# Kernel optimization log

Hardware: AMD Instinct MI355X
Metric: run time of the kernel (lower is better)

## Reference

```python
import jax, jax.numpy as jnp
import numpy as np

NEG_SLOPE = 0.2
EPS = 1e-16


def gat_layer(x, src, dst, W, att_src, att_dst, bias, heads, concat):
    N = x.shape[0]
    C = W.shape[1] // heads
    h = (x @ W).reshape(N, heads, C)                      # [N,H,C]
    a_src = (h * att_src).sum(-1)                         # [N,H]
    a_dst = (h * att_dst).sum(-1)                         # [N,H]
    e = jax.nn.leaky_relu(a_src[src] + a_dst[dst], NEG_SLOPE)  # [E,H]
    # numerically-stable softmax over incoming edges of each dst node
    e_max = jax.ops.segment_max(e, dst, num_segments=N)   # [N,H]
    e_max = jnp.where(jnp.isfinite(e_max), e_max, 0.0)
    ex = jnp.exp(e - e_max[dst])                          # [E,H]
    denom = jax.ops.segment_sum(ex, dst, num_segments=N) + EPS
    alpha = ex / denom[dst]                               # [E,H]
    msg = alpha[:, :, None] * h[src]                      # [E,H,C]
    out = jax.ops.segment_sum(msg, dst, num_segments=N)   # [N,H,C]
    if concat:
        return out.reshape(N, heads * C) + bias
    return out.mean(axis=1) + bias


def setup_inputs() -> dict:
    key = jax.random.key(0)
    ks = jax.random.split(key, 12)
    N, E = 50000, 800000
    IN, HID, OUT, H = 128, 8, 40, 8
    x = jax.random.normal(ks[0], (N, IN), dtype=jnp.float32)
    edge_index = jax.random.randint(ks[1], (2, E), 0, N, dtype=jnp.int64)
    s1 = 1.0 / np.sqrt(IN)
    s2 = 1.0 / np.sqrt(HID * H)
    W1 = jax.random.normal(ks[2], (IN, H * HID), dtype=jnp.float32) * s1
    att_src1 = jax.random.normal(ks[3], (H, HID), dtype=jnp.float32) * 0.1
    att_dst1 = jax.random.normal(ks[4], (H, HID), dtype=jnp.float32) * 0.1
    bias1 = jnp.zeros((H * HID,), dtype=jnp.float32)
    W2 = jax.random.normal(ks[5], (H * HID, OUT), dtype=jnp.float32) * s2
    att_src2 = jax.random.normal(ks[6], (1, OUT), dtype=jnp.float32) * 0.1
    att_dst2 = jax.random.normal(ks[7], (1, OUT), dtype=jnp.float32) * 0.1
    bias2 = jnp.zeros((OUT,), dtype=jnp.float32)
    return {"x": x, "edge_index": edge_index,
            "W1": W1, "att_src1": att_src1, "att_dst1": att_dst1, "bias1": bias1,
            "W2": W2, "att_src2": att_src2, "att_dst2": att_dst2, "bias2": bias2}


def reference(x, edge_index, W1, att_src1, att_dst1, bias1, W2, att_src2, att_dst2, bias2):
    src, dst = edge_index[0], edge_index[1]
    # eval mode: dropout is identity
    h = gat_layer(x, src, dst, W1, att_src1, att_dst1, bias1, heads=8, concat=True)
    h = jax.nn.elu(h)
    out = gat_layer(h, src, dst, W2, att_src2, att_dst2, bias2, heads=1, concat=False)
    return out
```

## Files before the change

### kernel.cpp

```cpp
#include <hip/hip_runtime.h>
#include <math.h>

#define EPS 1e-16f
#define SLOT 64
__device__ __forceinline__ float lrelu(float v) { return v > 0.0f ? v : 0.2f * v; }

__device__ __forceinline__ unsigned short f2bf(float f) {
    unsigned u = __float_as_uint(f);
    u += 0x7FFF + ((u >> 16) & 1);
    return (unsigned short)(u >> 16);
}
__device__ __forceinline__ float bf2f(unsigned short s) {
    return __uint_as_float(((unsigned)s) << 16);
}

__global__ void k_zero(int* __restrict__ deg, int N) {
    int i = blockIdx.x * 256 + threadIdx.x;
    if (i < N) deg[i] = 0;
}

#define LDK1 129
#define LDN1 65
__global__ __launch_bounds__(256, 2) void k_gemm1_scat(
    const float* __restrict__ x, const float* __restrict__ W1,
    const float* __restrict__ att_src1, const float* __restrict__ att_dst1,
    unsigned short* __restrict__ h1b, float* __restrict__ a_src1, float* __restrict__ a_dst1,
    int N, int D, const int* __restrict__ src, const int* __restrict__ dst,
    int* __restrict__ deg, int* __restrict__ ssrc, int E) {
    __shared__ float sX[64 * LDK1];
    __shared__ float sW[128 * LDN1];
    int t = threadIdx.x;
    if (blockIdx.x < D) {
        int e0 = (blockIdx.x * 256 + t) * 4;
        if (e0 < E) {
            int4 s4 = *((const int4*)(src + e0));
            int4 d4 = *((const int4*)(dst + e0));
            int p0 = atomicAdd(&deg[d4.x], 1);
            int p1 = atomicAdd(&deg[d4.y], 1);
            int p2 = atomicAdd(&deg[d4.z], 1);
            int p3 = atomicAdd(&deg[d4.w], 1);
            if (p0 < SLOT) ssrc[(d4.x << 6) + p0] = s4.x;
            if (p1 < SLOT) ssrc[(d4.y << 6) + p1] = s4.y;
            if (p2 < SLOT) ssrc[(d4.z << 6) + p2] = s4.z;
            if (p3 < SLOT) ssrc[(d4.w << 6) + p3] = s4.w;
        }
        return;
    }
    int r0 = (blockIdx.x - D) * 64;
    for (int i = t; i < 2048; i += 256) {
        int k = i >> 4, n4 = i & 15;
        float4 v = ((const float4*)W1)[i];
        float* p = sW + k * LDN1 + 4 * n4;
        p[0] = v.x; p[1] = v.y; p[2] = v.z; p[3] = v.w;
    }
    for (int i = t; i < 2048; i += 256) {
        int m = i >> 5, k4 = i & 31;
        int r = r0 + m;
        float4 v = make_float4(0.f, 0.f, 0.f, 0.f);
        if (r < N) v = ((const float4*)(x + (size_t)r * 128))[k4];
        float* p = sX + m * LDK1 + 4 * k4;
        p[0] = v.x; p[1] = v.y; p[2] = v.z; p[3] = v.w;
    }
    __syncthreads();
    int tx = t & 15, ty = t >> 4;
    const float* pA = sX + 4 * tx * LDK1;
    const float* pB = sW + 4 * ty;
    float c[4][4] = {{0.f}};
#pragma unroll 8
    for (int k = 0; k < 128; k++) {
        float a0 = pA[k], a1 = pA[LDK1 + k], a2 = pA[2 * LDK1 + k], a3 = pA[3 * LDK1 + k];
        const float* pb = pB + k * LDN1;
        float b0 = pb[0], b1 = pb[1], b2 = pb[2], b3 = pb[3];
        c[0][0] = fmaf(a0, b0, c[0][0]); c[0][1] = fmaf(a0, b1, c[0][1]);
        c[0][2] = fmaf(a0, b2, c[0][2]); c[0][3] = fmaf(a0, b3, c[0][3]);
        c[1][0] = fmaf(a1, b0, c[1][0]); c[1][1] = fmaf(a1, b1, c[1][1]);
        c[1][2] = fmaf(a1, b2, c[1][2]); c[1][3] = fmaf(a1, b3, c[1][3]);
        c[2][0] = fmaf(a2, b0, c[2][0]); c[2][1] = fmaf(a2, b1, c[2][1]);
        c[2][2] = fmaf(a2, b2, c[2][2]); c[2][3] = fmaf(a2, b3, c[2][3]);
        c[3][0] = fmaf(a3, b0, c[3][0]); c[3][1] = fmaf(a3, b1, c[3][1]);
        c[3][2] = fmaf(a3, b2, c[3][2]); c[3][3] = fmaf(a3, b3, c[3][3]);
    }
    float as0 = att_src1[4 * ty + 0], as1 = att_src1[4 * ty + 1],
          as2 = att_src1[4 * ty + 2], as3 = att_src1[4 * ty + 3];
    float ad0 = att_dst1[4 * ty + 0], ad1 = att_dst1[4 * ty + 1],
          ad2 = att_dst1[4 * ty + 2], ad3 = att_dst1[4 * ty + 3];
    __syncthreads();
    float* sPs = sX;
    float* sPd = sX + 64 * 17;
#pragma unroll
    for (int i = 0; i < 4; i++) {
        int row = 4 * tx + i;
        int r = r0 + row;
        if (r < N) {
            ushort4 hv;
            hv.x = f2bf(c[i][0]); hv.y = f2bf(c[i][1]);
            hv.z = f2bf(c[i][2]); hv.w = f2bf(c[i][3]);
            *((ushort4*)(h1b + (size_t)r * 64 + 4 * ty)) = hv;
        }
        sPs[row * 17 + ty] = fmaf(c[i][0], as0, fmaf(c[i][1], as1, fmaf(c[i][2], as2, c[i][3] * as3)));
        sPd[row * 17 + ty] = fmaf(c[i][0], ad0, fmaf(c[i][1], ad1, fmaf(c[i][2], ad2, c[i][3] * ad3)));
    }
    __syncthreads();
    for (int i = t; i < 512; i += 256) {
        int row = i >> 3, h = i & 7;
        int r = r0 + row;
        if (r < N) {
            a_src1[r * 8 + h] = sPs[row * 17 + 2 * h] + sPs[row * 17 + 2 * h + 1];
            a_dst1[r * 8 + h] = sPd[row * 17 + 2 * h] + sPd[row * 17 + 2 * h + 1];
        }
    }
}

__global__ __launch_bounds__(256) void k_node_agg1(
    const int* __restrict__ deg, const int* __restrict__ ssrc,
    const float* __restrict__ a_src1, const float* __restrict__ a_dst1,
    const unsigned short* __restrict__ h1b, const float* __restrict__ bias1,
    float* __restrict__ xx, int N) {
    int d = (blockIdx.x * 256 + threadIdx.x) >> 6;
    int lane = threadIdx.x & 63;
    if (d >= N) return;
    int start = d << 6;
    int end = start + min(deg[d], SLOT);
    int hcol = lane >> 3;
    int h8 = lane & 7;
    int eoff = lane >> 3;
    float adst8 = a_dst1[d * 8 + h8];
    float acc0 = 0.0f, acc1 = 0.0f, lsumA = 0.0f;
    int base = start;
    for (; base + 8 <= end; base += 8) {
        int s_l = ssrc[base + eoff];
        float ex_l = __expf(lrelu(a_src1[(size_t)s_l * 8 + h8] + adst8));
        lsumA += ex_l;
        int s0 = __shfl(s_l, 0),  s1 = __shfl(s_l, 8),  s2 = __shfl(s_l, 16), s3 = __shfl(s_l, 24);
        int s4 = __shfl(s_l, 32), s5 = __shfl(s_l, 40), s6 = __shfl(s_l, 48), s7 = __shfl(s_l, 56);
        float f0 = __shfl(ex_l, hcol),      f1 = __shfl(ex_l, 8 + hcol);
        float f2 = __shfl(ex_l, 16 + hcol), f3 = __shfl(ex_l, 24 + hcol);
        float f4 = __shfl(ex_l, 32 + hcol), f5 = __shfl(ex_l, 40 + hcol);
        float f6 = __shfl(ex_l, 48 + hcol), f7 = __shfl(ex_l, 56 + hcol);
        float g0 = bf2f(h1b[(size_t)s0 * 64 + lane]), g1 = bf2f(h1b[(size_t)s1 * 64 + lane]);
        float g2 = bf2f(h1b[(size_t)s2 * 64 + lane]), g3 = bf2f(h1b[(size_t)s3 * 64 + lane]);
        float g4 = bf2f(h1b[(size_t)s4 * 64 + lane]), g5 = bf2f(h1b[(size_t)s5 * 64 + lane]);
        float g6 = bf2f(h1b[(size_t)s6 * 64 + lane]), g7 = bf2f(h1b[(size_t)s7 * 64 + lane]);
        acc0 = fmaf(f0, g0, acc0); acc1 = fmaf(f1, g1, acc1);
        acc0 = fmaf(f2, g2, acc0); acc1 = fmaf(f3, g3, acc1);
        acc0 = fmaf(f4, g4, acc0); acc1 = fmaf(f5, g5, acc1);
        acc0 = fmaf(f6, g6, acc0); acc1 = fmaf(f7, g7, acc1);
    }
    int ecnt = end - base;
    if (ecnt > 0) {
        int s_l = 0; float ex_l = 0.0f;
        if (eoff < ecnt) {
            s_l = ssrc[base + eoff];
            ex_l = __expf(lrelu(a_src1[(size_t)s_l * 8 + h8] + adst8));
        }
        lsumA += ex_l;
        for (int j = 0; j < ecnt; j++) {
            int sj = __shfl(s_l, j * 8);
            float fj = __shfl(ex_l, j * 8 + hcol);
            acc0 = fmaf(fj, bf2f(h1b[(size_t)sj * 64 + lane]), acc0);
        }
    }
    float t = lsumA;
    t += __shfl_xor(t, 8); t += __shfl_xor(t, 16); t += __shfl_xor(t, 32);
    float lsum = __shfl(t, hcol);
    float o = (acc0 + acc1) / (lsum + EPS) + bias1[lane];
    xx[(size_t)d * 64 + lane] = o > 0.0f ? o : expm1f(o);
}

#define LDK2 65
#define LDN2 41
__global__ __launch_bounds__(256, 2) void k_gemm2(
    const float* __restrict__ xx, const float* __restrict__ W2,
    const float* __restrict__ att_src2, const float* __restrict__ att_dst2,
    float* __restrict__ h2, float* __restrict__ a_src2, float* __restrict__ a_dst2, int N) {
    __shared__ float sX[64 * LDK2];
    __shared__ float sW[64 * LDN2];
    int t = threadIdx.x;
    int r0 = blockIdx.x * 64;
    for (int i = t; i < 640; i += 256) {
        int k = i / 10, n4 = i - k * 10;
        float4 v = ((const float4*)W2)[i];
        float* p = sW + k * LDN2 + 4 * n4;
        p[0] = v.x; p[1] = v.y; p[2] = v.z; p[3] = v.w;
    }
    for (int i = t; i < 1024; i += 256) {
        int m = i >> 4, k4 = i & 15;
        int r = r0 + m;
        float4 v = make_float4(0.f, 0.f, 0.f, 0.f);
        if (r < N) v = ((const float4*)(xx + (size_t)r * 64))[k4];
        float* p = sX + m * LDK2 + 4 * k4;
        p[0] = v.x; p[1] = v.y; p[2] = v.z; p[3] = v.w;
    }
    __syncthreads();
    int tx = t & 15, ty = t >> 4;
    bool act = ty < 10;
    float c[4][4] = {{0.f}};
    if (act) {
        const float* pA = sX + 4 * tx * LDK2;
        const float* pB = sW + 4 * ty;
#pragma unroll 8
        for (int k = 0; k < 64; k++) {
            float a0 = pA[k], a1 = pA[LDK2 + k], a2 = pA[2 * LDK2 + k], a3 = pA[3 * LDK2 + k];
            const float* pb = pB + k * LDN2;
            float b0 = pb[0], b1 = pb[1], b2 = pb[2], b3 = pb[3];
            c[0][0] = fmaf(a0, b0, c[0][0]); c[0][1] = fmaf(a0, b1, c[0][1]);
            c[0][2] = fmaf(a0, b2, c[0][2]); c[0][3] = fmaf(a0, b3, c[0][3]);
            c[1][0] = fmaf(a1, b0, c[1][0]); c[1][1] = fmaf(a1, b1, c[1][1]);
            c[1][2] = fmaf(a1, b2, c[1][2]); c[1][3] = fmaf(a1, b3, c[1][3]);
            c[2][0] = fmaf(a2, b0, c[2][0]); c[2][1] = fmaf(a2, b1, c[2][1]);
            c[2][2] = fmaf(a2, b2, c[2][2]); c[2][3] = fmaf(a2, b3, c[2][3]);
            c[3][0] = fmaf(a3, b0, c[3][0]); c[3][1] = fmaf(a3, b1, c[3][1]);
            c[3][2] = fmaf(a3, b2, c[3][2]); c[3][3] = fmaf(a3, b3, c[3][3]);
        }
    }
    float as0 = 0.f, as1 = 0.f, as2 = 0.f, as3 = 0.f;
    float ad0 = 0.f, ad1 = 0.f, ad2 = 0.f, ad3 = 0.f;
    if (act) {
        as0 = att_src2[4 * ty + 0]; as1 = att_src2[4 * ty + 1];
        as2 = att_src2[4 * ty + 2]; as3 = att_src2[4 * ty + 3];
        ad0 = att_dst2[4 * ty + 0]; ad1 = att_dst2[4 * ty + 1];
        ad2 = att_dst2[4 * ty + 2]; ad3 = att_dst2[4 * ty + 3];
    }
    __syncthreads();
    float* sPs = sX;
    float* sPd = sX + 64 * 11;
#pragma unroll
    for (int i = 0; i < 4; i++) {
        int row = 4 * tx + i;
        int r = r0 + row;
        if (act) {
            if (r < N) {
                float4 hv = make_float4(c[i][0], c[i][1], c[i][2], c[i][3]);
                *((float4*)(h2 + (size_t)r * 40 + 4 * ty)) = hv;
            }
            sPs[row * 11 + ty] = fmaf(c[i][0], as0, fmaf(c[i][1], as1, fmaf(c[i][2], as2, c[i][3] * as3)));
            sPd[row * 11 + ty] = fmaf(c[i][0], ad0, fmaf(c[i][1], ad1, fmaf(c[i][2], ad2, c[i][3] * ad3)));
        }
    }
    __syncthreads();
    if (t < 64) {
        int r = r0 + t;
        if (r < N) {
            float ps = 0.f, pd = 0.f;
#pragma unroll
            for (int j = 0; j < 10; j++) {
                ps += sPs[t * 11 + j];
                pd += sPd[t * 11 + j];
            }
            a_src2[r] = ps;
            a_dst2[r] = pd;
        }
    }
}

__global__ __launch_bounds__(256) void k_node_agg2(
    const int* __restrict__ deg, const int* __restrict__ ssrc,
    const float* __restrict__ a_src2, const float* __restrict__ a_dst2,
    const float* __restrict__ h2, const float* __restrict__ bias2,
    float* __restrict__ out, int N) {
    int d = (blockIdx.x * 256 + threadIdx.x) >> 6;
    int lane = threadIdx.x & 63;
    if (d >= N) return;
    int start = d << 6;
    int end = start + min(deg[d], SLOT);
    float adst = a_dst2[d];
    bool act = lane < 40;
    float acc0 = 0.0f, acc1 = 0.0f, lsumA = 0.0f;
    for (int base = start; base < end; base += 64) {
        int ecnt = min(64, end - base);
        int s_l = 0; float ex_l = 0.0f;
        if (lane < ecnt) {
            s_l = ssrc[base + lane];
            ex_l = __expf(lrelu(a_src2[s_l] + adst));
        }
        lsumA += ex_l;
        int j = 0;
        for (; j + 8 <= ecnt; j += 8) {
            int s0 = __shfl(s_l, j),     s1 = __shfl(s_l, j + 1), s2 = __shfl(s_l, j + 2), s3 = __shfl(s_l, j + 3);
            int s4 = __shfl(s_l, j + 4), s5 = __shfl(s_l, j + 5), s6 = __shfl(s_l, j + 6), s7 = __shfl(s_l, j + 7);
            float f0 = __shfl(ex_l, j),     f1 = __shfl(ex_l, j + 1), f2 = __shfl(ex_l, j + 2), f3 = __shfl(ex_l, j + 3);
            float f4 = __shfl(ex_l, j + 4), f5 = __shfl(ex_l, j + 5), f6 = __shfl(ex_l, j + 6), f7 = __shfl(ex_l, j + 7);
            float g0 = act ? h2[(size_t)s0 * 40 + lane] : 0.0f;
            float g1 = act ? h2[(size_t)s1 * 40 + lane] : 0.0f;
            float g2 = act ? h2[(size_t)s2 * 40 + lane] : 0.0f;
            float g3 = act ? h2[(size_t)s3 * 40 + lane] : 0.0f;
            float g4 = act ? h2[(size_t)s4 * 40 + lane] : 0.0f;
            float g5 = act ? h2[(size_t)s5 * 40 + lane] : 0.0f;
            float g6 = act ? h2[(size_t)s6 * 40 + lane] : 0.0f;
            float g7 = act ? h2[(size_t)s7 * 40 + lane] : 0.0f;
            acc0 = fmaf(f0, g0, acc0); acc1 = fmaf(f1, g1, acc1);
            acc0 = fmaf(f2, g2, acc0); acc1 = fmaf(f3, g3, acc1);
            acc0 = fmaf(f4, g4, acc0); acc1 = fmaf(f5, g5, acc1);
            acc0 = fmaf(f6, g6, acc0); acc1 = fmaf(f7, g7, acc1);
        }
        for (; j < ecnt; j++) {
            int sj = __shfl(s_l, j);
            float fj = __shfl(ex_l, j);
            float g = act ? h2[(size_t)sj * 40 + lane] : 0.0f;
            acc0 = fmaf(fj, g, acc0);
        }
    }
    float t = lsumA;
#pragma unroll
    for (int off = 32; off; off >>= 1) t += __shfl_xor(t, off);
    if (act) out[(size_t)d * 40 + lane] = (acc0 + acc1) / (t + EPS) + bias2[lane];
}

extern "C" void kernel_launch(void* const* d_in, const int* in_sizes, int n_in,
                              void* d_out, int out_size, void* d_ws, size_t ws_size,
                              hipStream_t stream) {
    const float* x        = (const float*)d_in[0];
    const int*   ei       = (const int*)d_in[1];
    const float* W1       = (const float*)d_in[2];
    const float* att_src1 = (const float*)d_in[3];
    const float* att_dst1 = (const float*)d_in[4];
    const float* bias1    = (const float*)d_in[5];
    const float* W2       = (const float*)d_in[6];
    const float* att_src2 = (const float*)d_in[7];
    const float* att_dst2 = (const float*)d_in[8];
    const float* bias2    = (const float*)d_in[9];
    float* out = (float*)d_out;

    const int N = in_sizes[0] / 128;
    const int E = in_sizes[1] / 2;
    const int* src = ei;
    const int* dst = ei + E;

    float* ws = (float*)d_ws;
    size_t off = 0;
    int*   deg      = (int*)(ws + off); off += (size_t)N;
    int*   ssrc     = (int*)(ws + off); off += (size_t)N * SLOT;
    unsigned short* h1b = (unsigned short*)(ws + off); off += (size_t)N * 32;
    float* a_src1   = ws + off; off += (size_t)N * 8;
    float* a_dst1   = ws + off; off += (size_t)N * 8;
    float* xx       = ws + off; off += (size_t)N * 64;
    float* h2       = ws + off; off += (size_t)N * 40;
    float* a_src2   = ws + off; off += (size_t)N;
    float* a_dst2   = ws + off; off += (size_t)N;

    const int B = 256;
    auto g = [](int n) { return (n + 255) / 256; };
    int G1 = (N + 63) / 64;
    int D  = (E / 4 + 255) / 256;

    k_zero<<<g(N), B, 0, stream>>>(deg, N);
    k_gemm1_scat<<<D + G1, B, 0, stream>>>(x, W1, att_src1, att_dst1, h1b, a_src1, a_dst1,
                                           N, D, src, dst, deg, ssrc, E);
    k_node_agg1<<<(N + 3) / 4, B, 0, stream>>>(deg, ssrc, a_src1, a_dst1, h1b, bias1, xx, N);
    k_gemm2<<<G1, B, 0, stream>>>(xx, W2, att_src2, att_dst2, h2, a_src2, a_dst2, N);
    k_node_agg2<<<(N + 3) / 4, B, 0, stream>>>(deg, ssrc, a_src2, a_dst2, h2, bias2, out, N);
}
```

Before: 231.0 us.

## Partition edge scatter by destination range across eight block groups

The edge bucketing phase now launches eight groups of blocks. Each group reads every edge but only performs atomics and slot writes for destinations in its own eighth of the node range. The aim is to localize atomic and scatter traffic so that each group's writes hit a smaller region, which should help L2 locality. The cost is reading the edge list eight times and launching many more blocks that mostly skip their work.

```diff
diff --git a/kernel.cpp b/kernel.cpp
--- a/kernel.cpp
+++ b/kernel.cpp
@@ -31,18 +31,23 @@
     __shared__ float sW[128 * LDN1];
     int t = threadIdx.x;
     if (blockIdx.x < D) {
-        int e0 = (blockIdx.x * 256 + t) * 4;
+        int grp = blockIdx.x & 7;
+        int chunk = blockIdx.x >> 3;
+        int e0 = (chunk * 256 + t) * 8;
         if (e0 < E) {
-            int4 s4 = *((const int4*)(src + e0));
-            int4 d4 = *((const int4*)(dst + e0));
-            int p0 = atomicAdd(&deg[d4.x], 1);
-            int p1 = atomicAdd(&deg[d4.y], 1);
-            int p2 = atomicAdd(&deg[d4.z], 1);
-            int p3 = atomicAdd(&deg[d4.w], 1);
-            if (p0 < SLOT) ssrc[(d4.x << 6) + p0] = s4.x;
-            if (p1 < SLOT) ssrc[(d4.y << 6) + p1] = s4.y;
-            if (p2 < SLOT) ssrc[(d4.z << 6) + p2] = s4.z;
-            if (p3 < SLOT) ssrc[(d4.w << 6) + p3] = s4.w;
+            int lo = grp * N / 8, hi = (grp + 1) * N / 8;
+            int4 sa = *((const int4*)(src + e0));
+            int4 da = *((const int4*)(dst + e0));
+            int4 sb = *((const int4*)(src + e0 + 4));
+            int4 db = *((const int4*)(dst + e0 + 4));
+#define SCAT1(dd, ss)                                                   \
+            if ((dd) >= lo && (dd) < hi) {                              \
+                int p = atomicAdd(&deg[dd], 1);                         \
+                if (p < SLOT) ssrc[((dd) << 6) + p] = (ss);             \
+            }
+            SCAT1(da.x, sa.x) SCAT1(da.y, sa.y) SCAT1(da.z, sa.z) SCAT1(da.w, sa.w)
+            SCAT1(db.x, sb.x) SCAT1(db.y, sb.y) SCAT1(db.z, sb.z) SCAT1(db.w, sb.w)
+#undef SCAT1
         }
         return;
     }
@@ -341,7 +346,8 @@
     const int B = 256;
     auto g = [](int n) { return (n + 255) / 256; };
     int G1 = (N + 63) / 64;
-    int D  = (E / 4 + 255) / 256;
+    int C  = (E / 8 + 255) / 256;
+    int D  = 8 * C;
 
     k_zero<<<g(N), B, 0, stream>>>(deg, N);
     k_gemm1_scat<<<D + G1, B, 0, stream>>>(x, W1, att_src1, att_dst1, h1b, a_src1, a_dst1,
```

Result: slower. 238.1 us (+3.1%).

## Fuse layer-2 projection and attention logits into layer-1 aggregation kernel

Applied to the files above, without the earlier changes.

Removes the separate GEMM2 kernel and the xx intermediate buffer. After each wavefront computes its node's 64 ELU outputs, it broadcasts them with shuffles and multiplies by W2, which every block stages in shared memory. It then writes h2 and reduces a_src2 and a_dst2 with xor-shuffles. This saves a kernel launch and the global write and read of the 50000x64 intermediate. The cost is that every block reloads the 10 KB W2 into LDS, a barrier is added before aggregation, and there are 64 extra shuffles per node.

```diff
diff --git a/kernel.cpp b/kernel.cpp
--- a/kernel.cpp
+++ b/kernel.cpp
@@ -111,13 +111,19 @@
     }
 }
 
-__global__ __launch_bounds__(256) void k_node_agg1(
+__global__ __launch_bounds__(256) void k_node_agg1f(
     const int* __restrict__ deg, const int* __restrict__ ssrc,
     const float* __restrict__ a_src1, const float* __restrict__ a_dst1,
     const unsigned short* __restrict__ h1b, const float* __restrict__ bias1,
-    float* __restrict__ xx, int N) {
-    int d = (blockIdx.x * 256 + threadIdx.x) >> 6;
-    int lane = threadIdx.x & 63;
+    const float* __restrict__ W2, const float* __restrict__ att_src2,
+    const float* __restrict__ att_dst2,
+    float* __restrict__ h2, float* __restrict__ a_src2, float* __restrict__ a_dst2, int N) {
+    __shared__ float sW2[2560];
+    int t = threadIdx.x;
+    for (int i = t; i < 2560; i += 256) sW2[i] = W2[i];
+    __syncthreads();
+    int d = (blockIdx.x * 256 + t) >> 6;
+    int lane = t & 63;
     if (d >= N) return;
     int start = d << 6;
     int end = start + min(deg[d], SLOT);
@@ -160,97 +166,33 @@
             acc0 = fmaf(fj, bf2f(h1b[(size_t)sj * 64 + lane]), acc0);
         }
     }
-    float t = lsumA;
-    t += __shfl_xor(t, 8); t += __shfl_xor(t, 16); t += __shfl_xor(t, 32);
-    float lsum = __shfl(t, hcol);
+    float tr = lsumA;
+    tr += __shfl_xor(tr, 8); tr += __shfl_xor(tr, 16); tr += __shfl_xor(tr, 32);
+    float lsum = __shfl(tr, hcol);
     float o = (acc0 + acc1) / (lsum + EPS) + bias1[lane];
-    xx[(size_t)d * 64 + lane] = o > 0.0f ? o : expm1f(o);
-}
-
-#define LDK2 65
-#define LDN2 41
-__global__ __launch_bounds__(256, 2) void k_gemm2(
-    const float* __restrict__ xx, const float* __restrict__ W2,
-    const float* __restrict__ att_src2, const float* __restrict__ att_dst2,
-    float* __restrict__ h2, float* __restrict__ a_src2, float* __restrict__ a_dst2, int N) {
-    __shared__ float sX[64 * LDK2];
-    __shared__ float sW[64 * LDN2];
-    int t = threadIdx.x;
-    int r0 = blockIdx.x * 64;
-    for (int i = t; i < 640; i += 256) {
-        int k = i / 10, n4 = i - k * 10;
-        float4 v = ((const float4*)W2)[i];
-        float* p = sW + k * LDN2 + 4 * n4;
-        p[0] = v.x; p[1] = v.y; p[2] = v.z; p[3] = v.w;
-    }
-    for (int i = t; i < 1024; i += 256) {
-        int m = i >> 4, k4 = i & 15;
-        int r = r0 + m;
-        float4 v = make_float4(0.f, 0.f, 0.f, 0.f);
-        if (r < N) v = ((const float4*)(xx + (size_t)r * 64))[k4];
-        float* p = sX + m * LDK2 + 4 * k4;
-        p[0] = v.x; p[1] = v.y; p[2] = v.z; p[3] = v.w;
-    }
-    __syncthreads();
-    int tx = t & 15, ty = t >> 4;
-    bool act = ty < 10;
-    float c[4][4] = {{0.f}};
-    if (act) {
-        const float* pA = sX + 4 * tx * LDK2;
-        const float* pB = sW + 4 * ty;
-#pragma unroll 8
-        for (int k = 0; k < 64; k++) {
-            float a0 = pA[k], a1 = pA[LDK2 + k], a2 = pA[2 * LDK2 + k], a3 = pA[3 * LDK2 + k];
-            const float* pb = pB + k * LDN2;
-            float b0 = pb[0], b1 = pb[1], b2 = pb[2], b3 = pb[3];
-            c[0][0] = fmaf(a0, b0, c[0][0]); c[0][1] = fmaf(a0, b1, c[0][1]);
-            c[0][2] = fmaf(a0, b2, c[0][2]); c[0][3] = fmaf(a0, b3, c[0][3]);
-            c[1][0] = fmaf(a1, b0, c[1][0]); c[1][1] = fmaf(a1, b1, c[1][1]);
-            c[1][2] = fmaf(a1, b2, c[1][2]); c[1][3] = fmaf(a1, b3, c[1][3]);
-            c[2][0] = fmaf(a2, b0, c[2][0]); c[2][1] = fmaf(a2, b1, c[2][1]);
-            c[2][2] = fmaf(a2, b2, c[2][2]); c[2][3] = fmaf(a2, b3, c[2][3]);
-            c[3][0] = fmaf(a3, b0, c[3][0]); c[3][1] = fmaf(a3, b1, c[3][1]);
-            c[3][2] = fmaf(a3, b2, c[3][2]); c[3][3] = fmaf(a3, b3, c[3][3]);
-        }
-    }
-    float as0 = 0.f, as1 = 0.f, as2 = 0.f, as3 = 0.f;
-    float ad0 = 0.f, ad1 = 0.f, ad2 = 0.f, ad3 = 0.f;
-    if (act) {
-        as0 = att_src2[4 * ty + 0]; as1 = att_src2[4 * ty + 1];
-        as2 = att_src2[4 * ty + 2]; as3 = att_src2[4 * ty + 3];
-        ad0 = att_dst2[4 * ty + 0]; ad1 = att_dst2[4 * ty + 1];
-        ad2 = att_dst2[4 * ty + 2]; ad3 = att_dst2[4 * ty + 3];
-    }
-    __syncthreads();
-    float* sPs = sX;
-    float* sPd = sX + 64 * 11;
-#pragma unroll
-    for (int i = 0; i < 4; i++) {
-        int row = 4 * tx + i;
-        int r = r0 + row;
-        if (act) {
-            if (r < N) {
-                float4 hv = make_float4(c[i][0], c[i][1], c[i][2], c[i][3]);
-                *((float4*)(h2 + (size_t)r * 40 + 4 * ty)) = hv;
-            }
-            sPs[row * 11 + ty] = fmaf(c[i][0], as0, fmaf(c[i][1], as1, fmaf(c[i][2], as2, c[i][3] * as3)));
-            sPd[row * 11 + ty] = fmaf(c[i][0], ad0, fmaf(c[i][1], ad1, fmaf(c[i][2], ad2, c[i][3] * ad3)));
-        }
-    }
-    __syncthreads();
-    if (t < 64) {
-        int r = r0 + t;
-        if (r < N) {
-            float ps = 0.f, pd = 0.f;
-#pragma unroll
-            for (int j = 0; j < 10; j++) {
-                ps += sPs[t * 11 + j];
-                pd += sPd[t * 11 + j];
-            }
-            a_src2[r] = ps;
-            a_dst2[r] = pd;
-        }
-    }
+    o = o > 0.0f ? o : expm1f(o);
+    int jj = lane < 40 ? lane : 39;
+    float hj0 = 0.f, hj1 = 0.f, hj2 = 0.f, hj3 = 0.f;
+#pragma unroll
+    for (int l = 0; l < 64; l += 4) {
+        float x0 = __shfl(o, l),     x1 = __shfl(o, l + 1);
+        float x2 = __shfl(o, l + 2), x3 = __shfl(o, l + 3);
+        hj0 = fmaf(x0, sW2[(l + 0) * 40 + jj], hj0);
+        hj1 = fmaf(x1, sW2[(l + 1) * 40 + jj], hj1);
+        hj2 = fmaf(x2, sW2[(l + 2) * 40 + jj], hj2);
+        hj3 = fmaf(x3, sW2[(l + 3) * 40 + jj], hj3);
+    }
+    float hj = (hj0 + hj1) + (hj2 + hj3);
+    bool actj = lane < 40;
+    if (actj) h2[(size_t)d * 40 + lane] = hj;
+    float ps = actj ? hj * att_src2[lane] : 0.f;
+    float pd = actj ? hj * att_dst2[lane] : 0.f;
+#pragma unroll
+    for (int off = 32; off; off >>= 1) {
+        ps += __shfl_xor(ps, off);
+        pd += __shfl_xor(pd, off);
+    }
+    if (lane == 0) { a_src2[d] = ps; a_dst2[d] = pd; }
 }
 
 __global__ __launch_bounds__(256) void k_node_agg2(
@@ -333,7 +275,6 @@
     unsigned short* h1b = (unsigned short*)(ws + off); off += (size_t)N * 32;
     float* a_src1   = ws + off; off += (size_t)N * 8;
     float* a_dst1   = ws + off; off += (size_t)N * 8;
-    float* xx       = ws + off; off += (size_t)N * 64;
     float* h2       = ws + off; off += (size_t)N * 40;
     float* a_src2   = ws + off; off += (size_t)N;
     float* a_dst2   = ws + off; off += (size_t)N;
@@ -346,7 +287,7 @@
     k_zero<<<g(N), B, 0, stream>>>(deg, N);
     k_gemm1_scat<<<D + G1, B, 0, stream>>>(x, W1, att_src1, att_dst1, h1b, a_src1, a_dst1,
                                            N, D, src, dst, deg, ssrc, E);
-    k_node_agg1<<<(N + 3) / 4, B, 0, stream>>>(deg, ssrc, a_src1, a_dst1, h1b, bias1, xx, N);
-    k_gemm2<<<G1, B, 0, stream>>>(xx, W2, att_src2, att_dst2, h2, a_src2, a_dst2, N);
+    k_node_agg1f<<<(N + 3) / 4, B, 0, stream>>>(deg, ssrc, a_src1, a_dst1, h1b, bias1,
+                                                W2, att_src2, att_dst2, h2, a_src2, a_dst2, N);
     k_node_agg2<<<(N + 3) / 4, B, 0, stream>>>(deg, ssrc, a_src2, a_dst2, h2, bias2, out, N);
 }
```

Result: slower. 267.0 us (+15.6%).
